# Optimization experiments

Hardware: AMD Instinct MI355X
Metric: run time of the kernel (lower is better)

## Reference

```python
import jax, jax.numpy as jnp
import numpy as np


def _sobel_filters():
    # 3D Sobel kernels for x, y, z directions, shape (3, 1, 3, 3, 3) in OIDHW.
    x = np.array([[[-1, 0, 1], [-2, 0, 2], [-1, 0, 1]],
                  [[-2, 0, 2], [-4, 0, 4], [-2, 0, 2]],
                  [[-1, 0, 1], [-2, 0, 2], [-1, 0, 1]]], dtype=np.float32)
    y = np.array([[[1, 2, 1], [0, 0, 0], [-1, -2, -1]],
                  [[2, 4, 2], [0, 0, 0], [-2, -4, -2]],
                  [[1, 2, 1], [0, 0, 0], [-1, -2, -1]]], dtype=np.float32)
    z = np.array([[[1, 2, 1], [2, 4, 2], [1, 2, 1]],
                  [[0, 0, 0], [0, 0, 0], [0, 0, 0]],
                  [[-1, -2, -1], [-2, -4, -2], [-1, -2, -1]]], dtype=np.float32)
    return jnp.asarray(np.stack([x, y, z])[:, None])  # (3,1,3,3,3)


_FILTERS = _sobel_filters()
_EPS = 1e-10


def gradient3d(x):
    # x: [B,1,D,H,W] -> gradient magnitude [B,1,D,H,W].
    # Single conv with 3 output channels == three separate torch conv3d + concat.
    g = jax.lax.conv_general_dilated(
        x, _FILTERS, window_strides=(1, 1, 1),
        padding=[(1, 1), (1, 1), (1, 1)],
        dimension_numbers=('NCDHW', 'OIDHW', 'NCDHW'))  # [B,3,D,H,W]
    return jnp.sqrt(jnp.sum(g * g, axis=1, keepdims=True) + _EPS)


def setup_inputs() -> dict:
    key = jax.random.key(0)
    k1, k2, k3 = jax.random.split(key, 3)
    shape = (2, 1, 192, 192, 192)
    pred = jax.random.normal(k1, shape, dtype=jnp.float32)
    gt_dose = jax.random.normal(k2, shape, dtype=jnp.float32)
    body_mask = (jax.random.uniform(k3, shape) > 0.3).astype(jnp.float32)
    return {"pred": pred, "gt_dose": gt_dose, "body_mask": body_mask}


def reference(pred, gt_dose, body_mask):
    mse = jnp.square(pred - gt_dose) * body_mask
    mge = jnp.square(gradient3d(gt_dose) - gradient3d(pred)) * body_mask
    return jnp.mean(mse + jnp.tanh(mge) * mse)
```

## Files before the change

kernel.cpp:

```cpp
#include <hip/hip_runtime.h>
#include <math.h>

#define W 192
#define H 192
#define DEPTH 192
#define BATCH 2
#define TW 64
#define TH 8
#define DC 12
#define HW (H * W)
#define VOL ((size_t)DEPTH * HW)
#define LROW 72
#define LPLANE (LROW * 10)
#define NPAIR ((DC + 2) / 2)
#define NITEM 720

__global__ __launch_bounds__(256) void sobel_loss_part(
    const float* __restrict__ pred, const float* __restrict__ gt,
    const float* __restrict__ mask, float* __restrict__ partials)
{
    __shared__ __align__(16) float lds[2 * 2 * LPLANE];

    const int tid = threadIdx.x;
    const int tx = blockIdx.x % 3;
    const int ty = blockIdx.x / 3;
    const int w0 = tx * TW, h0 = ty * TH;
    const int d0 = blockIdx.y * DC;
    const size_t base = (size_t)blockIdx.z * VOL;

    const int wy  = tid >> 5;
    const int wxo = (tid & 31) << 1;
    const size_t moff = base + (size_t)(h0 + wy) * W + (w0 + wxo);

    int it_ok[3], it_st[3], it_q[3], it_lds[3];
    size_t it_goff[3];
    const float* it_src[3];
    #pragma unroll
    for (int k = 0; k < 3; ++k) {
        int j = tid + 256 * k;
        int jj = (j < NITEM) ? j : 0;
        int a = jj / 360; int pj = jj - a * 360;
        int q = pj / 180; int e = pj - q * 180;
        int r = e / 18;   int c = e - r * 18;
        int y  = h0 - 1 + r;
        int xf = w0 - 4 + 4 * c;
        it_st[k]  = (j < NITEM);
        it_ok[k]  = it_st[k] && ((unsigned)y < (unsigned)H) && ((unsigned)xf < (unsigned)W);
        it_goff[k] = it_ok[k] ? ((size_t)y * W + xf) : 0;
        it_lds[k]  = ((a * 2 + q) * 10 + r) * LROW + 4 * c;
        it_q[k]    = q;
        it_src[k]  = a ? gt : pred;
    }

    float4 R[3];
    auto load_pair = [&](int s) {
        const int p0 = d0 - 1 + 2 * s;
        #pragma unroll
        for (int k = 0; k < 3; ++k) {
            const int p = p0 + it_q[k];
            const bool v = it_ok[k] && (p >= 0) && (p < DEPTH);
            R[k] = v ? *(const float4*)(it_src[k] + base + (size_t)p * HW + it_goff[k])
                     : make_float4(0.f, 0.f, 0.f, 0.f);
        }
    };

    float2 Mn = make_float2(0.f, 0.f), Mn1 = make_float2(0.f, 0.f);
    float2 Mc, Mc1;
    auto load_mask = [&](int s) {
        Mn  = *(const float2*)(mask + moff + (size_t)(d0 + 2 * s - 2) * HW);
        Mn1 = *(const float2*)(mask + moff + (size_t)(d0 + 2 * s - 1) * HW);
    };

    float dx[2][2][3], dy[2][2][3], sm[2][2][3], ct[2][2][2];
    #pragma unroll
    for (int a = 0; a < 2; ++a)
        #pragma unroll
        for (int o = 0; o < 2; ++o) {
            dx[a][o][0]=dx[a][o][1]=dx[a][o][2]=0.f;
            dy[a][o][0]=dy[a][o][1]=dy[a][o][2]=0.f;
            sm[a][o][0]=sm[a][o][1]=sm[a][o][2]=0.f;
            ct[a][o][0]=ct[a][o][1]=0.f;
        }
    float acc = 0.f;

    load_pair(0);

    for (int s = 0; s < NPAIR; ++s) {
        __syncthreads();
        #pragma unroll
        for (int k = 0; k < 3; ++k)
            if (it_st[k]) *(float4*)(lds + it_lds[k]) = R[k];
        __syncthreads();

        Mc = Mn; Mc1 = Mn1;
        if (s + 1 < NPAIR) {
            load_pair(s + 1);
            load_mask(s + 1);
        }

        #pragma unroll
        for (int q = 0; q < 2; ++q) {
            const int p = d0 - 1 + 2 * s + q;
            float e[2][3][4];
            #pragma unroll
            for (int a = 0; a < 2; ++a)
                #pragma unroll
                for (int r = 0; r < 3; ++r)
                    #pragma unroll
                    for (int c = 0; c < 4; ++c)
                        e[a][r][c] = lds[(a * 2 + q) * LPLANE + (wy + r) * LROW + wxo + 3 + c];

            #pragma unroll
            for (int a = 0; a < 2; ++a)
                #pragma unroll
                for (int o = 0; o < 2; ++o) {
                    float s0 = e[a][0][o] + 2.f * e[a][0][o+1] + e[a][0][o+2];
                    float s1 = e[a][1][o] + 2.f * e[a][1][o+1] + e[a][1][o+2];
                    float s2 = e[a][2][o] + 2.f * e[a][2][o+1] + e[a][2][o+2];
                    float dd0 = e[a][0][o+2] - e[a][0][o];
                    float dd1 = e[a][1][o+2] - e[a][1][o];
                    float dd2 = e[a][2][o+2] - e[a][2][o];
                    dx[a][o][0] = dx[a][o][1]; dx[a][o][1] = dx[a][o][2]; dx[a][o][2] = dd0 + 2.f * dd1 + dd2;
                    sm[a][o][0] = sm[a][o][1]; sm[a][o][1] = sm[a][o][2]; sm[a][o][2] = s0 + 2.f * s1 + s2;
                    dy[a][o][0] = dy[a][o][1]; dy[a][o][1] = dy[a][o][2]; dy[a][o][2] = s0 - s2;
                    ct[a][o][0] = ct[a][o][1]; ct[a][o][1] = e[a][1][o+1];
                }

            if (p >= d0 + 1) {
                const float2 M = q ? Mc1 : Mc;
                #pragma unroll
                for (int o = 0; o < 2; ++o) {
                    float gxa = dx[0][o][0] + 2.f * dx[0][o][1] + dx[0][o][2];
                    float gya = dy[0][o][0] + 2.f * dy[0][o][1] + dy[0][o][2];
                    float gza = sm[0][o][0] - sm[0][o][2];
                    float gxb = dx[1][o][0] + 2.f * dx[1][o][1] + dx[1][o][2];
                    float gyb = dy[1][o][0] + 2.f * dy[1][o][1] + dy[1][o][2];
                    float gzb = sm[1][o][0] - sm[1][o][2];
                    float ga = __builtin_amdgcn_sqrtf(gxa * gxa + gya * gya + gza * gza + 1e-10f);
                    float gb = __builtin_amdgcn_sqrtf(gxb * gxb + gyb * gyb + gzb * gzb + 1e-10f);
                    float m  = o ? M.y : M.x;
                    float dm = ct[0][o][0] - ct[1][o][0];
                    float mse = dm * dm * m;
                    float dg  = gb - ga;
                    float mge = dg * dg * m;
                    float ex = __expf(2.f * mge);
                    float t  = 1.f - 2.f * __builtin_amdgcn_rcpf(ex + 1.f);
                    acc += mse * (1.f + t);
                }
            }
        }
    }

    float v = acc;
    #pragma unroll
    for (int o = 32; o > 0; o >>= 1) v += __shfl_down(v, o, 64);
    __shared__ float red[4];
    if ((tid & 63) == 0) red[tid >> 6] = v;
    __syncthreads();
    if (tid == 0) {
        partials[(size_t)blockIdx.z * (gridDim.x * gridDim.y)
                 + (size_t)blockIdx.y * gridDim.x + blockIdx.x]
            = red[0] + red[1] + red[2] + red[3];
    }
}

__global__ __launch_bounds__(256) void reduce_final(
    const float* __restrict__ partials, int n, float* __restrict__ out)
{
    int tid = threadIdx.x;
    double s = 0.0;
    for (int i = tid; i < n; i += 256) s += (double)partials[i];
    #pragma unroll
    for (int o = 32; o > 0; o >>= 1) s += __shfl_down(s, o, 64);
    __shared__ double red[4];
    if ((tid & 63) == 0) red[tid >> 6] = s;
    __syncthreads();
    if (tid == 0) {
        double t = red[0] + red[1] + red[2] + red[3];
        const double ntot = (double)BATCH * (double)DEPTH * (double)H * (double)W;
        out[0] = (float)(t / ntot);
    }
}

extern "C" void kernel_launch(void* const* d_in, const int* in_sizes, int n_in,
                              void* d_out, int out_size, void* d_ws, size_t ws_size,
                              hipStream_t stream) {
    const float* pred = (const float*)d_in[0];
    const float* gt   = (const float*)d_in[1];
    const float* mask = (const float*)d_in[2];
    float* partials = (float*)d_ws;

    dim3 grid((W / TW) * (H / TH), DEPTH / DC, BATCH);
    sobel_loss_part<<<grid, 256, 0, stream>>>(pred, gt, mask, partials);

    int nparts = grid.x * grid.y * grid.z;
    reduce_final<<<1, 256, 0, stream>>>(partials, nparts, (float*)d_out);
}
```

Baseline: 185.6 us.

## Precompute horizontal Sobel passes before LDS store and use ring-buffer registers

Each thread now loads a float4 plus its left and right neighbour scalars and computes the x-direction smooth and difference terms before writing to LDS. Each output column's pair is stored packed, so the compute phase reads three float4s per volume instead of twelve scalars. Depth history moves to a modular ring buffer with a fully unrolled loop, which replaces the register shifting. Center pred and gt values are reloaded from global memory rather than kept in registers, and the tanh epilogue is folded into FMAs. In exchange this issues more small uncoalesced scalar global loads and adds extra center loads.

Measured after the change: 186.6 us. No clear change (+0.6%).

```diff
diff --git a/kernel.cpp b/kernel.cpp
--- a/kernel.cpp
+++ b/kernel.cpp
@@ -10,142 +10,163 @@
 #define DC 12
 #define HW (H * W)
 #define VOL ((size_t)DEPTH * HW)
-#define LROW 72
-#define LPLANE (LROW * 10)
-#define NPAIR ((DC + 2) / 2)
-#define NITEM 720
+#define NPAIR 7
+#define LROW 128
+#define LPL (10 * LROW)
+#define NUNIT 640
+
 
 __global__ __launch_bounds__(256) void sobel_loss_part(
     const float* __restrict__ pred, const float* __restrict__ gt,
     const float* __restrict__ mask, float* __restrict__ partials)
 {
-    __shared__ __align__(16) float lds[2 * 2 * LPLANE];
+    __shared__ __align__(16) float lds[4 * LPL];
 
     const int tid = threadIdx.x;
-    const int tx = blockIdx.x % 3;
-    const int ty = blockIdx.x / 3;
+    const int tx = blockIdx.x % 3, ty = blockIdx.x / 3;
     const int w0 = tx * TW, h0 = ty * TH;
     const int d0 = blockIdx.y * DC;
     const size_t base = (size_t)blockIdx.z * VOL;
 
     const int wy  = tid >> 5;
     const int wxo = (tid & 31) << 1;
-    const size_t moff = base + (size_t)(h0 + wy) * W + (w0 + wxo);
-
-    int it_ok[3], it_st[3], it_q[3], it_lds[3];
-    size_t it_goff[3];
-    const float* it_src[3];
+    const size_t coff = base + (size_t)(h0 + wy) * W + (w0 + wxo);
+
+    int u_st[3], u_rowok[3], u_lok[3], u_rok[3], u_q[3], u_lds[3];
+    size_t u_goff[3];
+    const float* u_src[3];
     #pragma unroll
     for (int k = 0; k < 3; ++k) {
-        int j = tid + 256 * k;
-        int jj = (j < NITEM) ? j : 0;
-        int a = jj / 360; int pj = jj - a * 360;
-        int q = pj / 180; int e = pj - q * 180;
-        int r = e / 18;   int c = e - r * 18;
-        int y  = h0 - 1 + r;
-        int xf = w0 - 4 + 4 * c;
-        it_st[k]  = (j < NITEM);
-        it_ok[k]  = it_st[k] && ((unsigned)y < (unsigned)H) && ((unsigned)xf < (unsigned)W);
-        it_goff[k] = it_ok[k] ? ((size_t)y * W + xf) : 0;
-        it_lds[k]  = ((a * 2 + q) * 10 + r) * LROW + 4 * c;
-        it_q[k]    = q;
-        it_src[k]  = a ? gt : pred;
-    }
-
-    float4 R[3];
+        int u = tid + 256 * k;
+        int uu = (u < NUNIT) ? u : 0;
+        int a = uu / 320; int rem = uu - a * 320;
+        int q = rem / 160; int rem2 = rem - q * 160;
+        int r = rem2 >> 4; int cg = rem2 & 15;
+        int y = h0 - 1 + r;
+        int x = w0 + 4 * cg;
+        u_st[k]    = (u < NUNIT);
+        u_rowok[k] = u_st[k] && ((unsigned)y < (unsigned)H);
+        u_lok[k]   = (x > 0);
+        u_rok[k]   = (x + 4 < W);
+        u_goff[k]  = u_rowok[k] ? ((size_t)y * W + x) : 0;
+        u_q[k]     = q;
+        u_lds[k]   = ((a * 2 + q) * 10 + r) * LROW + cg * 8;
+        u_src[k]   = a ? gt : pred;
+    }
+
+    float4 X[3]; float XL[3], XR[3];
     auto load_pair = [&](int s) {
         const int p0 = d0 - 1 + 2 * s;
         #pragma unroll
         for (int k = 0; k < 3; ++k) {
-            const int p = p0 + it_q[k];
-            const bool v = it_ok[k] && (p >= 0) && (p < DEPTH);
-            R[k] = v ? *(const float4*)(it_src[k] + base + (size_t)p * HW + it_goff[k])
-                     : make_float4(0.f, 0.f, 0.f, 0.f);
+            const int p = p0 + u_q[k];
+            const bool ok = u_rowok[k] && (p >= 0) && (p < DEPTH);
+            const float* sp = u_src[k] + base + (size_t)p * HW + u_goff[k];
+            X[k]  = ok ? *(const float4*)sp : make_float4(0.f, 0.f, 0.f, 0.f);
+            XL[k] = (ok && u_lok[k]) ? sp[-1] : 0.f;
+            XR[k] = (ok && u_rok[k]) ? sp[4]  : 0.f;
         }
     };
 
-    float2 Mn = make_float2(0.f, 0.f), Mn1 = make_float2(0.f, 0.f);
-    float2 Mc, Mc1;
-    auto load_mask = [&](int s) {
-        Mn  = *(const float2*)(mask + moff + (size_t)(d0 + 2 * s - 2) * HW);
-        Mn1 = *(const float2*)(mask + moff + (size_t)(d0 + 2 * s - 1) * HW);
+    float2 Mn = {0,0}, Mn1 = {0,0}, Pn = {0,0}, Pn1 = {0,0}, Gn = {0,0}, Gn1 = {0,0};
+    auto load_ctr = [&](int s) {
+        size_t o0 = coff + (size_t)(d0 + 2 * s - 2) * HW;
+        size_t o1 = coff + (size_t)(d0 + 2 * s - 1) * HW;
+        Mn  = *(const float2*)(mask + o0);  Mn1 = *(const float2*)(mask + o1);
+        Pn  = *(const float2*)(pred + o0);  Pn1 = *(const float2*)(pred + o1);
+        Gn  = *(const float2*)(gt   + o0);  Gn1 = *(const float2*)(gt   + o1);
     };
 
-    float dx[2][2][3], dy[2][2][3], sm[2][2][3], ct[2][2][2];
+    float hdx[2][2][3], hsx[2][2][3], hdy[2][2][3];
     #pragma unroll
     for (int a = 0; a < 2; ++a)
         #pragma unroll
-        for (int o = 0; o < 2; ++o) {
-            dx[a][o][0]=dx[a][o][1]=dx[a][o][2]=0.f;
-            dy[a][o][0]=dy[a][o][1]=dy[a][o][2]=0.f;
-            sm[a][o][0]=sm[a][o][1]=sm[a][o][2]=0.f;
-            ct[a][o][0]=ct[a][o][1]=0.f;
-        }
+        for (int o = 0; o < 2; ++o)
+            #pragma unroll
+            for (int j = 0; j < 3; ++j) { hdx[a][o][j] = 0.f; hsx[a][o][j] = 0.f; hdy[a][o][j] = 0.f; }
     float acc = 0.f;
 
     load_pair(0);
 
+    #pragma unroll
     for (int s = 0; s < NPAIR; ++s) {
         __syncthreads();
         #pragma unroll
-        for (int k = 0; k < 3; ++k)
-            if (it_st[k]) *(float4*)(lds + it_lds[k]) = R[k];
+        for (int k = 0; k < 3; ++k) {
+            if (u_st[k]) {
+                float4 x4 = X[k]; float xl = XL[k], xr = XR[k];
+                float4 w1, w2;
+                w1.x = xl   + 2.f * x4.x + x4.y;  w1.y = x4.y - xl;
+                w1.z = x4.x + 2.f * x4.y + x4.z;  w1.w = x4.z - x4.x;
+                w2.x = x4.y + 2.f * x4.z + x4.w;  w2.y = x4.w - x4.y;
+                w2.z = x4.z + 2.f * x4.w + xr;    w2.w = xr   - x4.z;
+                *(float4*)(lds + u_lds[k])     = w1;
+                *(float4*)(lds + u_lds[k] + 4) = w2;
+            }
+        }
         __syncthreads();
 
-        Mc = Mn; Mc1 = Mn1;
-        if (s + 1 < NPAIR) {
-            load_pair(s + 1);
-            load_mask(s + 1);
-        }
+        float2 Mc0 = Mn, Mc1 = Mn1, Pc0 = Pn, Pc1 = Pn1, Gc0 = Gn, Gc1 = Gn1;
+        if (s + 1 < NPAIR) { load_pair(s + 1); load_ctr(s + 1); }
 
         #pragma unroll
         for (int q = 0; q < 2; ++q) {
-            const int p = d0 - 1 + 2 * s + q;
-            float e[2][3][4];
+            const int t = 2 * s + q;
+            const int wsl = t % 3;
+            const int i0  = (t + 1) % 3;
+            const int i1  = (t + 2) % 3;
+            const int i2  = wsl;
+
+            const float* LA = lds + (q * 10 + wy) * LROW + wxo * 2;
+            const float* LB = lds + ((2 + q) * 10 + wy) * LROW + wxo * 2;
+            float4 A0 = *(const float4*)(LA);
+            float4 A1 = *(const float4*)(LA + LROW);
+            float4 A2 = *(const float4*)(LA + 2 * LROW);
+            float4 B0 = *(const float4*)(LB);
+            float4 B1 = *(const float4*)(LB + LROW);
+            float4 B2 = *(const float4*)(LB + 2 * LROW);
+
             #pragma unroll
-            for (int a = 0; a < 2; ++a)
-                #pragma unroll
-                for (int r = 0; r < 3; ++r)
-                    #pragma unroll
-                    for (int c = 0; c < 4; ++c)
-                        e[a][r][c] = lds[(a * 2 + q) * LPLANE + (wy + r) * LROW + wxo + 3 + c];
-
-            #pragma unroll
-            for (int a = 0; a < 2; ++a)
+            for (int o = 0; o < 2; ++o) {
+                float sA0 = o ? A0.z : A0.x, dA0 = o ? A0.w : A0.y;
+                float sA1 = o ? A1.z : A1.x, dA1 = o ? A1.w : A1.y;
+                float sA2 = o ? A2.z : A2.x, dA2 = o ? A2.w : A2.y;
+                hdx[0][o][wsl] = dA0 + 2.f * dA1 + dA2;
+                hsx[0][o][wsl] = sA0 + 2.f * sA1 + sA2;
+                hdy[0][o][wsl] = sA0 - sA2;
+                float sB0 = o ? B0.z : B0.x, dB0 = o ? B0.w : B0.y;
+                float sB1 = o ? B1.z : B1.x, dB1 = o ? B1.w : B1.y;
+                float sB2 = o ? B2.z : B2.x, dB2 = o ? B2.w : B2.y;
+                hdx[1][o][wsl] = dB0 + 2.f * dB1 + dB2;
+                hsx[1][o][wsl] = sB0 + 2.f * sB1 + sB2;
+                hdy[1][o][wsl] = sB0 - sB2;
+            }
+
+            if (t >= 2) {
+                const float2 M = q ? Mc1 : Mc0;
+                const float2 P = q ? Pc1 : Pc0;
+                const float2 G = q ? Gc1 : Gc0;
                 #pragma unroll
                 for (int o = 0; o < 2; ++o) {
-                    float s0 = e[a][0][o] + 2.f * e[a][0][o+1] + e[a][0][o+2];
-                    float s1 = e[a][1][o] + 2.f * e[a][1][o+1] + e[a][1][o+2];
-                    float s2 = e[a][2][o] + 2.f * e[a][2][o+1] + e[a][2][o+2];
-                    float dd0 = e[a][0][o+2] - e[a][0][o];
-                    float dd1 = e[a][1][o+2] - e[a][1][o];
-                    float dd2 = e[a][2][o+2] - e[a][2][o];
-                    dx[a][o][0] = dx[a][o][1]; dx[a][o][1] = dx[a][o][2]; dx[a][o][2] = dd0 + 2.f * dd1 + dd2;
-                    sm[a][o][0] = sm[a][o][1]; sm[a][o][1] = sm[a][o][2]; sm[a][o][2] = s0 + 2.f * s1 + s2;
-                    dy[a][o][0] = dy[a][o][1]; dy[a][o][1] = dy[a][o][2]; dy[a][o][2] = s0 - s2;
-                    ct[a][o][0] = ct[a][o][1]; ct[a][o][1] = e[a][1][o+1];
-                }
-
-            if (p >= d0 + 1) {
-                const float2 M = q ? Mc1 : Mc;
-                #pragma unroll
-                for (int o = 0; o < 2; ++o) {
-                    float gxa = dx[0][o][0] + 2.f * dx[0][o][1] + dx[0][o][2];
-                    float gya = dy[0][o][0] + 2.f * dy[0][o][1] + dy[0][o][2];
-                    float gza = sm[0][o][0] - sm[0][o][2];
-                    float gxb = dx[1][o][0] + 2.f * dx[1][o][1] + dx[1][o][2];
-                    float gyb = dy[1][o][0] + 2.f * dy[1][o][1] + dy[1][o][2];
-                    float gzb = sm[1][o][0] - sm[1][o][2];
-                    float ga = __builtin_amdgcn_sqrtf(gxa * gxa + gya * gya + gza * gza + 1e-10f);
-                    float gb = __builtin_amdgcn_sqrtf(gxb * gxb + gyb * gyb + gzb * gzb + 1e-10f);
+                    float gx = hdx[0][o][i0] + 2.f * hdx[0][o][i1] + hdx[0][o][i2];
+                    float gy = hdy[0][o][i0] + 2.f * hdy[0][o][i1] + hdy[0][o][i2];
+                    float gz = hsx[0][o][i0] - hsx[0][o][i2];
+                    float ga = __builtin_amdgcn_sqrtf(
+                        fmaf(gz, gz, fmaf(gy, gy, fmaf(gx, gx, 1e-10f))));
+                    float hx = hdx[1][o][i0] + 2.f * hdx[1][o][i1] + hdx[1][o][i2];
+                    float hy = hdy[1][o][i0] + 2.f * hdy[1][o][i1] + hdy[1][o][i2];
+                    float hz = hsx[1][o][i0] - hsx[1][o][i2];
+                    float gb = __builtin_amdgcn_sqrtf(
+                        fmaf(hz, hz, fmaf(hy, hy, fmaf(hx, hx, 1e-10f))));
                     float m  = o ? M.y : M.x;
-                    float dm = ct[0][o][0] - ct[1][o][0];
+                    float dm = (o ? P.y : P.x) - (o ? G.y : G.x);
                     float mse = dm * dm * m;
                     float dg  = gb - ga;
                     float mge = dg * dg * m;
-                    float ex = __expf(2.f * mge);
-                    float t  = 1.f - 2.f * __builtin_amdgcn_rcpf(ex + 1.f);
-                    acc += mse * (1.f + t);
+                    float ex = __expf(mge + mge);
+                    float rc = __builtin_amdgcn_rcpf(ex + 1.f);
+                    float c  = fmaf(-2.f, rc, 2.f);
+                    acc = fmaf(mse, c, acc);
                 }
             }
         }
```
